# Performance work log

Hardware: AMD Instinct MI355X
Metric: run time of the kernel (lower is better)

The kernel has to match this reference:

```python
import jax, jax.numpy as jnp
import numpy as np


def _pe_2d(H, W, C, dtype):
    # PositionalEncodingPermute2D: returns (C, H, W)
    ch_half = (C + 1) // 2
    inv = 1.0 / (10000.0 ** (jnp.arange(0, ch_half, 2, dtype=jnp.float32) / ch_half))
    tH = jnp.arange(H, dtype=jnp.float32)
    tW = jnp.arange(W, dtype=jnp.float32)
    sinH = tH[:, None] * inv[None, :]              # (H, ch_half//2)
    sinW = tW[:, None] * inv[None, :]              # (W, ch_half//2)
    embH = jnp.concatenate([jnp.sin(sinH), jnp.cos(sinH)], axis=-1)  # (H, ch_half)
    embW = jnp.concatenate([jnp.sin(sinW), jnp.cos(sinW)], axis=-1)  # (W, ch_half)
    E = jnp.concatenate([
        jnp.broadcast_to(embW[None, :, :], (H, W, ch_half)),
        jnp.broadcast_to(embH[:, None, :], (H, W, ch_half)),
    ], axis=-1)[..., :C]                            # (H, W, C)
    return jnp.transpose(E, (2, 0, 1)).astype(dtype)  # (C, H, W)


def setup_inputs() -> dict:
    key = jax.random.key(0)
    k0, k1, k2, k3 = jax.random.split(key, 4)
    B, C, H, W = 4, 256, 64, 64
    s = 1.0 / np.sqrt(C)  # kaiming-ish scale
    return {
        "x": jax.random.normal(k0, (B, C, H, W), dtype=jnp.float32),
        "wq": jax.random.normal(k1, (C, C), dtype=jnp.float32) * s,
        "wk": jax.random.normal(k2, (C, C), dtype=jnp.float32) * s,
        "wv": jax.random.normal(k3, (C, C), dtype=jnp.float32) * s,
    }


def reference(x, wq, wk, wv):
    B, C, H, W = x.shape
    scale = C ** (-0.5)
    x = x + _pe_2d(H, W, C, x.dtype)[None]          # (B, C, H, W)
    X = x.reshape(B, C, H * W).transpose(0, 2, 1)   # (B, N, C)
    Q = jnp.einsum('bnc,dc->bnd', X, wq)
    K = jnp.einsum('bnc,dc->bnd', X, wk)
    V = jnp.einsum('bnc,dc->bnd', X, wv)
    A = jax.nn.softmax(jnp.einsum('bnd,bmd->bnm', Q, K) * scale, axis=-1)
    Y = jnp.einsum('bnm,bmd->bnd', A, V)            # (B, N, C)
    return Y.transpose(0, 2, 1).reshape(B, C, H, W)
```

## Files before the change

### kernel.cpp

```cpp
#include <hip/hip_runtime.h>
#include <hip/hip_bf16.h>

#define BB 4
#define CC 256
#define NN 4096
#define NSPLIT 4
#define KSPLIT (NN / NSPLIT)
#define NPAIR (KSPLIT / 64)

typedef __attribute__((ext_vector_type(8))) short short8;
typedef __attribute__((ext_vector_type(4))) float floatx4;
typedef __attribute__((ext_vector_type(4))) unsigned short ushortx4;

__device__ __forceinline__ float bf2f(unsigned short u) {
  union { unsigned int i; float f; } cv; cv.i = ((unsigned int)u) << 16; return cv.f;
}
__device__ __forceinline__ unsigned short f2bf(float f) {
  union { __hip_bfloat16 h; unsigned short u; } cv; cv.h = __float2bfloat16(f); return cv.u;
}
__device__ __forceinline__ unsigned int cvtpk_bf16(float lo, float hi) {
  unsigned int r;
  asm("v_cvt_pk_bf16_f32 %0, %1, %2" : "=v"(r) : "v"(lo), "v"(hi));
  return r;
}

#define MFMA(a, b, c) __builtin_amdgcn_mfma_f32_16x16x32_bf16((a), (b), (c), 0, 0, 0)

__device__ __forceinline__ void dma16(const unsigned short* g, unsigned short* l) {
  __builtin_amdgcn_global_load_lds(
      (const __attribute__((address_space(1))) unsigned int*)g,
      (__attribute__((address_space(3))) unsigned int*)l, 16, 0, 0);
}
#define S_BARRIER __builtin_amdgcn_s_barrier()
#define MEMFENCE __asm__ volatile("" ::: "memory")

__global__ __launch_bounds__(256) void wcvt(const float* __restrict__ w0,
                                            const float* __restrict__ w1,
                                            const float* __restrict__ w2,
                                            unsigned short* __restrict__ o0,
                                            unsigned short* __restrict__ o1,
                                            unsigned short* __restrict__ o2,
                                            float* __restrict__ PEt) {
  if (blockIdx.y == 3) {
    int idx = blockIdx.x * 256 + threadIdx.x;
    int c = idx >> 6, p = idx & 63, j = c & 63;
    float freq = exp2f(-0.2076205059304601f * (float)j);
    float arg = (float)p * freq;
    PEt[idx] = (c & 64) ? cosf(arg) : sinf(arg);
    return;
  }
  const float* w = (blockIdx.y == 0) ? w0 : (blockIdx.y == 1) ? w1 : w2;
  unsigned short* o = (blockIdx.y == 0) ? o0 : (blockIdx.y == 1) ? o1 : o2;
  float s = (blockIdx.y == 0) ? 0.0901684400555590f : 1.0f;
  int i = (blockIdx.x * 256 + threadIdx.x) * 4;
  floatx4 v = *(const floatx4*)&w[i];
  ushortx4 p;
#pragma unroll
  for (int r = 0; r < 4; r++) p[r] = f2bf(v[r] * s);
  *(ushortx4*)&o[i] = p;
}

__global__ __launch_bounds__(256) void prep_x(const float* __restrict__ x,
                                              const float* __restrict__ PEt,
                                              unsigned short* __restrict__ Xbf) {
  __shared__ float tile[32][33];
  int b = blockIdx.z;
  int n0 = blockIdx.x * 32, c0 = blockIdx.y * 32;
  int tx = threadIdx.x, ty = threadIdx.y;
#pragma unroll
  for (int i = 0; i < 4; i++) {
    int c = c0 + ty + i * 8;
    int n = n0 + tx;
    float v = x[((long)(b * CC + c)) * NN + n];
    int hh = n >> 6, ww = n & 63;
    v += PEt[(c << 6) | ((c < 128) ? ww : hh)];
    tile[ty + i * 8][tx] = v;
  }
  __syncthreads();
#pragma unroll
  for (int i = 0; i < 4; i++) {
    int n = n0 + ty + i * 8;
    int c = c0 + tx;
    Xbf[((long)(b * NN + n)) * CC + c] = f2bf(tile[tx][ty + i * 8]);
  }
}

__global__ __launch_bounds__(256, 2) void gemm_fused(const unsigned short* __restrict__ Xbf,
                                                     const unsigned short* __restrict__ Wqk,
                                                     const unsigned short* __restrict__ Wv,
                                                     unsigned short* __restrict__ QK,
                                                     unsigned short* __restrict__ Vt) {
  __shared__ alignas(16) unsigned short Af[2][8 * 512];
  __shared__ alignas(16) unsigned short Bf[2][8 * 512];
  const unsigned short *Ab, *Bb;
  unsigned short* Ob;
  long row0, col0;
  int ldo;
  int F = blockIdx.x;
  if (F < 512) {
    int b = F >> 7, r = F & 127;
    row0 = (long)(r >> 2) * 128;
    col0 = (long)(r & 3) * 128;
    Ab = Xbf + (long)b * NN * CC;
    Bb = Wqk;
    Ob = QK + (long)b * NN * 512;
    ldo = 512;
  } else {
    int F2 = F - 512;
    int b = F2 >> 6, r = F2 & 63;
    row0 = (long)(r >> 5) * 128;
    col0 = (long)(r & 31) * 128;
    Ab = Wv;
    Bb = Xbf + (long)b * NN * CC;
    Ob = Vt + (long)b * CC * NN;
    ldo = NN;
  }
  int t = threadIdx.x, wave = t >> 6, lane = t & 63, quad = lane >> 4, l15 = lane & 15;
  int wr = wave >> 1, wc = wave & 1;

  auto stage = [&](int k0, int buf) {
#pragma unroll
    for (int i = 0; i < 2; i++) {
      int fg = wave * 2 + i;
      dma16(&Ab[(row0 + fg * 16 + l15) * 256 + k0 + quad * 8], &Af[buf][fg * 512]);
      dma16(&Bb[(col0 + fg * 16 + l15) * 256 + k0 + quad * 8], &Bf[buf][fg * 512]);
    }
  };

  floatx4 acc[4][4] = {};
  stage(0, 0);
  MEMFENCE;
#pragma unroll
  for (int ki = 0; ki < 8; ki++) {
    int buf = ki & 1;
    S_BARRIER;
    MEMFENCE;
    if (ki + 1 < 8) {
      stage((ki + 1) * 32, buf ^ 1);
      MEMFENCE;
      __builtin_amdgcn_s_waitcnt(0xF74);
    } else {
      __builtin_amdgcn_s_waitcnt(0xF70);
    }
    S_BARRIER;
    MEMFENCE;
    short8 af[4], bf[4];
#pragma unroll
    for (int i = 0; i < 4; i++) {
      af[i] = *(const short8*)&Af[buf][(wr * 4 + i) * 512 + lane * 8];
      bf[i] = *(const short8*)&Bf[buf][(wc * 4 + i) * 512 + lane * 8];
    }
#pragma unroll
    for (int i = 0; i < 4; i++)
#pragma unroll
      for (int j = 0; j < 4; j++) acc[i][j] = MFMA(af[i], bf[j], acc[i][j]);
  }

#pragma unroll
  for (int i = 0; i < 4; i++)
#pragma unroll
    for (int j = 0; j < 4; j++) {
      long col = col0 + (wc * 4 + j) * 16 + l15;
#pragma unroll
      for (int r = 0; r < 4; r++) {
        long row = row0 + (wr * 4 + i) * 16 + quad * 4 + r;
        Ob[row * (long)ldo + col] = f2bf(acc[i][j][r]);
      }
    }
}

__global__ __launch_bounds__(512) void attn(const unsigned short* __restrict__ QKg,
                                            const unsigned short* __restrict__ Vtg,
                                            unsigned short* __restrict__ Opart,
                                            float* __restrict__ Lp) {
  __shared__ alignas(16) unsigned short Kl[4 * 8192];
  __shared__ alignas(16) unsigned short Vl[4 * 8192];
  int F = blockIdx.x;
  int c = F & 15, sp = c & 3, b = c >> 2;
  long q0 = (long)(F >> 4) * 256;
  int t = threadIdx.x, wave = t >> 6, lane = t & 63, quad = lane >> 4, l15 = lane & 15;
  const unsigned short* Qb = QKg + (long)b * NN * 512;
  const unsigned short* Kb = Qb + 256;
  const unsigned short* Vb = Vtg + (long)b * CC * NN;

  short8 qf[2][8];
#pragma unroll
  for (int qb = 0; qb < 2; qb++) {
    long qrow = q0 + wave * 32 + qb * 16 + l15;
#pragma unroll
    for (int ks = 0; ks < 8; ks++)
      qf[qb][ks] = *(const short8*)&Qb[qrow * 512 + ks * 32 + quad * 8];
  }

  floatx4 acc[2][16] = {};
  float rs[2] = {0.f, 0.f};

  const int idx0 = (((lane >> 4) & 1) << 7) | ((lane & 15) << 2);
  const int idx1 = idx0 + 64;
  const bool lo32 = lane < 32;

  const int kbeg = sp * KSPLIT;

  auto stage_pair = [&](int p, int buf) {
#pragma unroll
    for (int tt = 0; tt < 2; tt++) {
      int m0 = kbeg + (p * 2 + tt) * 32;
      int slot = buf * 2 + tt;
#pragma unroll
      for (int st = 0; st < 2; st++) {
        int fg = st * 8 + wave;
        dma16(&Kb[(long)(m0 + st * 16 + l15) * 512 + wave * 32 + quad * 8],
              &Kl[slot * 8192 + fg * 512]);
        dma16(&Vb[(long)(fg * 16 + l15) * NN + m0 + quad * 8],
              &Vl[slot * 8192 + fg * 512]);
      }
    }
  };

  __builtin_amdgcn_s_waitcnt(0xF70);
  stage_pair(0, 0);
  MEMFENCE;

  for (int p = 0; p < NPAIR; p++) {
    int buf = p & 1;
    S_BARRIER;
    MEMFENCE;
    if (p + 1 < NPAIR) {
      stage_pair(p + 1, buf ^ 1);
      MEMFENCE;
      __builtin_amdgcn_s_waitcnt(0xF78);
    } else {
      __builtin_amdgcn_s_waitcnt(0xF70);
    }
    S_BARRIER;
    MEMFENCE;

#pragma unroll
    for (int tt = 0; tt < 2; tt++) {
      int kb = (buf * 2 + tt) * 8192;
      floatx4 s2[2][2];
      {
        floatx4 z = {0.f, 0.f, 0.f, 0.f};
        s2[0][0] = z; s2[0][1] = z; s2[1][0] = z; s2[1][1] = z;
      }
      __builtin_amdgcn_s_setprio(1);
#pragma unroll
      for (int fgk = 0; fgk < 16; fgk++) {
        short8 kf = *(const short8*)&Kl[kb + fgk * 512 + lane * 8];
        int mt = fgk >> 3, ks = fgk & 7;
        s2[0][mt] = MFMA(kf, qf[0][ks], s2[0][mt]);
        s2[1][mt] = MFMA(kf, qf[1][ks], s2[1][mt]);
      }
      __builtin_amdgcn_s_setprio(0);

      unsigned int pw[2][2][2];
#pragma unroll
      for (int qb = 0; qb < 2; qb++)
#pragma unroll
        for (int mt = 0; mt < 2; mt++) {
          float e0 = __builtin_amdgcn_exp2f(s2[qb][mt][0]);
          float e1 = __builtin_amdgcn_exp2f(s2[qb][mt][1]);
          float e2 = __builtin_amdgcn_exp2f(s2[qb][mt][2]);
          float e3 = __builtin_amdgcn_exp2f(s2[qb][mt][3]);
          rs[qb] += (e0 + e1) + (e2 + e3);
          pw[qb][mt][0] = cvtpk_bf16(e0, e1);
          pw[qb][mt][1] = cvtpk_bf16(e2, e3);
        }

      short8 pf[2];
#pragma unroll
      for (int qb = 0; qb < 2; qb++) {
        unsigned int x0 = (unsigned int)__builtin_amdgcn_ds_bpermute(idx0, (int)pw[qb][0][0]);
        unsigned int y0 = (unsigned int)__builtin_amdgcn_ds_bpermute(idx0, (int)pw[qb][1][0]);
        unsigned int x1 = (unsigned int)__builtin_amdgcn_ds_bpermute(idx0, (int)pw[qb][0][1]);
        unsigned int y1 = (unsigned int)__builtin_amdgcn_ds_bpermute(idx0, (int)pw[qb][1][1]);
        unsigned int x2 = (unsigned int)__builtin_amdgcn_ds_bpermute(idx1, (int)pw[qb][0][0]);
        unsigned int y2 = (unsigned int)__builtin_amdgcn_ds_bpermute(idx1, (int)pw[qb][1][0]);
        unsigned int x3 = (unsigned int)__builtin_amdgcn_ds_bpermute(idx1, (int)pw[qb][0][1]);
        unsigned int y3 = (unsigned int)__builtin_amdgcn_ds_bpermute(idx1, (int)pw[qb][1][1]);
        union { unsigned int u[4]; short8 s; } pk;
        pk.u[0] = lo32 ? x0 : y0;
        pk.u[1] = lo32 ? x1 : y1;
        pk.u[2] = lo32 ? x2 : y2;
        pk.u[3] = lo32 ? x3 : y3;
        pf[qb] = pk.s;
      }

      __builtin_amdgcn_s_setprio(1);
#pragma unroll
      for (int db = 0; db < 16; db++) {
        short8 vf = *(const short8*)&Vl[kb + db * 512 + lane * 8];
        acc[0][db] = MFMA(pf[0], vf, acc[0][db]);
        acc[1][db] = MFMA(pf[1], vf, acc[1][db]);
      }
      __builtin_amdgcn_s_setprio(0);
    }
  }

  unsigned short* Ob = Opart + (long)(b * NSPLIT + sp) * CC * NN;
#pragma unroll
  for (int qb = 0; qb < 2; qb++) {
    long nidx = q0 + wave * 32 + qb * 16 + quad * 4;
#pragma unroll
    for (int db = 0; db < 16; db++) {
      long d = db * 16 + l15;
      ushortx4 pk;
#pragma unroll
      for (int r = 0; r < 4; r++) pk[r] = f2bf(acc[qb][db][r]);
      *(ushortx4*)&Ob[d * NN + nidx] = pk;
    }
    float v = rs[qb];
    v += __shfl_xor(v, 16, 64);
    v += __shfl_xor(v, 32, 64);
    if (quad == 0)
      Lp[(long)(b * NSPLIT + sp) * NN + q0 + wave * 32 + qb * 16 + l15] = v;
  }
}

__global__ __launch_bounds__(256) void combine(const unsigned short* __restrict__ Op,
                                               const float* __restrict__ Lp,
                                               float* __restrict__ Out) {
  __shared__ float Wl[64];
  int b = blockIdx.z;
  int d0 = blockIdx.y * 64, n0 = blockIdx.x * 64;
  int t = threadIdx.x;
  if (t < 64) {
    int n = n0 + t;
    float L = 0.f;
#pragma unroll
    for (int s = 0; s < NSPLIT; s++) L += Lp[(long)(b * NSPLIT + s) * NN + n];
    Wl[t] = 1.0f / L;
  }
  __syncthreads();
  int tn = t & 15, td = t >> 4;
  int nb = n0 + tn * 4;
  float w[4];
#pragma unroll
  for (int r = 0; r < 4; r++) w[r] = Wl[tn * 4 + r];
#pragma unroll
  for (int dd = 0; dd < 4; dd++) {
    int d = d0 + td * 4 + dd;
    floatx4 o = {0.f, 0.f, 0.f, 0.f};
#pragma unroll
    for (int s = 0; s < NSPLIT; s++) {
      ushortx4 pv = *(const ushortx4*)&Op[((long)(b * NSPLIT + s) * CC + d) * NN + nb];
#pragma unroll
      for (int r = 0; r < 4; r++) o[r] += bf2f(pv[r]);
    }
#pragma unroll
    for (int r = 0; r < 4; r++) o[r] *= w[r];
    *(floatx4*)&Out[((long)b * CC + d) * NN + nb] = o;
  }
}

extern "C" void kernel_launch(void* const* d_in, const int* in_sizes, int n_in,
                              void* d_out, int out_size, void* d_ws, size_t ws_size,
                              hipStream_t stream) {
  const float* x = (const float*)d_in[0];
  const float* wq = (const float*)d_in[1];
  const float* wk = (const float*)d_in[2];
  const float* wv = (const float*)d_in[3];
  float* out = (float*)d_out;

  char* ws = (char*)d_ws;
  unsigned short* QKbuf = (unsigned short*)(ws);
  unsigned short* Vt = (unsigned short*)(ws + (16l << 20));
  unsigned short* Xbf = (unsigned short*)(ws + (24l << 20));
  unsigned short* Opart = (unsigned short*)(ws + (24l << 20));
  float* Lp = (float*)(ws + (56l << 20));
  unsigned short* Wqk = (unsigned short*)(ws + (57l << 20));
  unsigned short* Wv = (unsigned short*)(ws + (57l << 20) + (1 << 19));
  float* PEt = (float*)(ws + (57l << 20) + (3 << 18));

  wcvt<<<dim3(CC * CC / 1024, 4), 256, 0, stream>>>(wq, wk, wv, Wqk, Wqk + CC * CC, Wv, PEt);
  prep_x<<<dim3(NN / 32, CC / 32, BB), dim3(32, 8), 0, stream>>>(x, PEt, Xbf);
  gemm_fused<<<dim3(768), 256, 0, stream>>>(Xbf, Wqk, Wv, QKbuf, Vt);
  attn<<<dim3(256), 512, 0, stream>>>(QKbuf, Vt, Opart, Lp);
  combine<<<dim3(NN / 64, CC / 64, BB), 256, 0, stream>>>(Opart, Lp, out);
}
```

Measured before the change: 191.5 us.

## Split attention into 256-thread blocks of 128 queries with two blocks per CU

The attention kernel now uses 4-wave blocks covering 128 queries instead of 8-wave blocks covering 256. The grid grows to 512 blocks with launch bounds allowing two blocks per CU. Shared memory is halved to a plain double buffer of single 32-key tiles instead of pairs, and each wave stages two K/V fragment groups. Scheduling fences are added around the barriers and waits. The aim is better CU occupancy and overlap across independent blocks, at the cost of loading each K/V tile twice as often from global memory or L2 and tighter register limits.

```diff
diff --git a/kernel.cpp b/kernel.cpp
--- a/kernel.cpp
+++ b/kernel.cpp
@@ -6,7 +6,7 @@
 #define NN 4096
 #define NSPLIT 4
 #define KSPLIT (NN / NSPLIT)
-#define NPAIR (KSPLIT / 64)
+#define NT (KSPLIT / 32)
 
 typedef __attribute__((ext_vector_type(8))) short short8;
 typedef __attribute__((ext_vector_type(4))) float floatx4;
@@ -33,6 +33,7 @@
 }
 #define S_BARRIER __builtin_amdgcn_s_barrier()
 #define MEMFENCE __asm__ volatile("" ::: "memory")
+#define SCHED_FENCE __builtin_amdgcn_sched_barrier(0)
 
 __global__ __launch_bounds__(256) void wcvt(const float* __restrict__ w0,
                                             const float* __restrict__ w1,
@@ -169,15 +170,16 @@
     }
 }
 
-__global__ __launch_bounds__(512) void attn(const unsigned short* __restrict__ QKg,
-                                            const unsigned short* __restrict__ Vtg,
-                                            unsigned short* __restrict__ Opart,
-                                            float* __restrict__ Lp) {
-  __shared__ alignas(16) unsigned short Kl[4 * 8192];
-  __shared__ alignas(16) unsigned short Vl[4 * 8192];
+__global__ __launch_bounds__(256, 2) void attn(const unsigned short* __restrict__ QKg,
+                                               const unsigned short* __restrict__ Vtg,
+                                               unsigned short* __restrict__ Opart,
+                                               float* __restrict__ Lp) {
+  __shared__ alignas(16) unsigned short Kl[2 * 8192];
+  __shared__ alignas(16) unsigned short Vl[2 * 8192];
   int F = blockIdx.x;
-  int c = F & 15, sp = c & 3, b = c >> 2;
-  long q0 = (long)(F >> 4) * 256;
+  int c = F >> 5, qt = F & 31;
+  int sp = c & 3, b = c >> 2;
+  long q0 = (long)qt * 128;
   int t = threadIdx.x, wave = t >> 6, lane = t & 63, quad = lane >> 4, l15 = lane & 15;
   const unsigned short* Qb = QKg + (long)b * NN * 512;
   const unsigned short* Kb = Qb + 256;
@@ -201,100 +203,105 @@
 
   const int kbeg = sp * KSPLIT;
 
-  auto stage_pair = [&](int p, int buf) {
-#pragma unroll
-    for (int tt = 0; tt < 2; tt++) {
-      int m0 = kbeg + (p * 2 + tt) * 32;
-      int slot = buf * 2 + tt;
-#pragma unroll
-      for (int st = 0; st < 2; st++) {
-        int fg = st * 8 + wave;
-        dma16(&Kb[(long)(m0 + st * 16 + l15) * 512 + wave * 32 + quad * 8],
-              &Kl[slot * 8192 + fg * 512]);
+  auto stageT = [&](int tt) {
+    int m0 = kbeg + tt * 32;
+    int kb = (tt & 1) * 8192;
+#pragma unroll
+    for (int st = 0; st < 2; st++) {
+#pragma unroll
+      for (int i = 0; i < 2; i++) {
+        int d = wave * 2 + i;
+        int fg = st * 8 + d;
+        dma16(&Kb[(long)(m0 + st * 16 + l15) * 512 + d * 32 + quad * 8],
+              &Kl[kb + fg * 512]);
         dma16(&Vb[(long)(fg * 16 + l15) * NN + m0 + quad * 8],
-              &Vl[slot * 8192 + fg * 512]);
+              &Vl[kb + fg * 512]);
       }
     }
   };
 
-  __builtin_amdgcn_s_waitcnt(0xF70);
-  stage_pair(0, 0);
   MEMFENCE;
-
-  for (int p = 0; p < NPAIR; p++) {
-    int buf = p & 1;
+  __builtin_amdgcn_s_waitcnt(0x070);
+  SCHED_FENCE;
+  MEMFENCE;
+  stageT(0);
+  MEMFENCE;
+
+#pragma unroll 1
+  for (int tt = 0; tt < NT; tt++) {
     S_BARRIER;
     MEMFENCE;
-    if (p + 1 < NPAIR) {
-      stage_pair(p + 1, buf ^ 1);
+    SCHED_FENCE;
+    if (tt + 1 < NT) {
+      stageT(tt + 1);
       MEMFENCE;
       __builtin_amdgcn_s_waitcnt(0xF78);
     } else {
       __builtin_amdgcn_s_waitcnt(0xF70);
     }
+    SCHED_FENCE;
     S_BARRIER;
     MEMFENCE;
-
-#pragma unroll
-    for (int tt = 0; tt < 2; tt++) {
-      int kb = (buf * 2 + tt) * 8192;
-      floatx4 s2[2][2];
-      {
-        floatx4 z = {0.f, 0.f, 0.f, 0.f};
-        s2[0][0] = z; s2[0][1] = z; s2[1][0] = z; s2[1][1] = z;
+    SCHED_FENCE;
+
+    int kb = (tt & 1) * 8192;
+
+    floatx4 s2[2][2];
+    {
+      floatx4 z = {0.f, 0.f, 0.f, 0.f};
+      s2[0][0] = z; s2[0][1] = z; s2[1][0] = z; s2[1][1] = z;
+    }
+    __builtin_amdgcn_s_setprio(1);
+#pragma unroll
+    for (int fgk = 0; fgk < 16; fgk++) {
+      short8 kf = *(const short8*)&Kl[kb + fgk * 512 + lane * 8];
+      int mt = fgk >> 3, ks = fgk & 7;
+      s2[0][mt] = MFMA(kf, qf[0][ks], s2[0][mt]);
+      s2[1][mt] = MFMA(kf, qf[1][ks], s2[1][mt]);
+    }
+    __builtin_amdgcn_s_setprio(0);
+
+    unsigned int pw[2][2][2];
+#pragma unroll
+    for (int qb = 0; qb < 2; qb++)
+#pragma unroll
+      for (int mt = 0; mt < 2; mt++) {
+        float e0 = __builtin_amdgcn_exp2f(s2[qb][mt][0]);
+        float e1 = __builtin_amdgcn_exp2f(s2[qb][mt][1]);
+        float e2 = __builtin_amdgcn_exp2f(s2[qb][mt][2]);
+        float e3 = __builtin_amdgcn_exp2f(s2[qb][mt][3]);
+        rs[qb] += (e0 + e1) + (e2 + e3);
+        pw[qb][mt][0] = cvtpk_bf16(e0, e1);
+        pw[qb][mt][1] = cvtpk_bf16(e2, e3);
       }
-      __builtin_amdgcn_s_setprio(1);
-#pragma unroll
-      for (int fgk = 0; fgk < 16; fgk++) {
-        short8 kf = *(const short8*)&Kl[kb + fgk * 512 + lane * 8];
-        int mt = fgk >> 3, ks = fgk & 7;
-        s2[0][mt] = MFMA(kf, qf[0][ks], s2[0][mt]);
-        s2[1][mt] = MFMA(kf, qf[1][ks], s2[1][mt]);
-      }
-      __builtin_amdgcn_s_setprio(0);
-
-      unsigned int pw[2][2][2];
-#pragma unroll
-      for (int qb = 0; qb < 2; qb++)
-#pragma unroll
-        for (int mt = 0; mt < 2; mt++) {
-          float e0 = __builtin_amdgcn_exp2f(s2[qb][mt][0]);
-          float e1 = __builtin_amdgcn_exp2f(s2[qb][mt][1]);
-          float e2 = __builtin_amdgcn_exp2f(s2[qb][mt][2]);
-          float e3 = __builtin_amdgcn_exp2f(s2[qb][mt][3]);
-          rs[qb] += (e0 + e1) + (e2 + e3);
-          pw[qb][mt][0] = cvtpk_bf16(e0, e1);
-          pw[qb][mt][1] = cvtpk_bf16(e2, e3);
-        }
-
-      short8 pf[2];
-#pragma unroll
-      for (int qb = 0; qb < 2; qb++) {
-        unsigned int x0 = (unsigned int)__builtin_amdgcn_ds_bpermute(idx0, (int)pw[qb][0][0]);
-        unsigned int y0 = (unsigned int)__builtin_amdgcn_ds_bpermute(idx0, (int)pw[qb][1][0]);
-        unsigned int x1 = (unsigned int)__builtin_amdgcn_ds_bpermute(idx0, (int)pw[qb][0][1]);
-        unsigned int y1 = (unsigned int)__builtin_amdgcn_ds_bpermute(idx0, (int)pw[qb][1][1]);
-        unsigned int x2 = (unsigned int)__builtin_amdgcn_ds_bpermute(idx1, (int)pw[qb][0][0]);
-        unsigned int y2 = (unsigned int)__builtin_amdgcn_ds_bpermute(idx1, (int)pw[qb][1][0]);
-        unsigned int x3 = (unsigned int)__builtin_amdgcn_ds_bpermute(idx1, (int)pw[qb][0][1]);
-        unsigned int y3 = (unsigned int)__builtin_amdgcn_ds_bpermute(idx1, (int)pw[qb][1][1]);
-        union { unsigned int u[4]; short8 s; } pk;
-        pk.u[0] = lo32 ? x0 : y0;
-        pk.u[1] = lo32 ? x1 : y1;
-        pk.u[2] = lo32 ? x2 : y2;
-        pk.u[3] = lo32 ? x3 : y3;
-        pf[qb] = pk.s;
-      }
-
-      __builtin_amdgcn_s_setprio(1);
-#pragma unroll
-      for (int db = 0; db < 16; db++) {
-        short8 vf = *(const short8*)&Vl[kb + db * 512 + lane * 8];
-        acc[0][db] = MFMA(pf[0], vf, acc[0][db]);
-        acc[1][db] = MFMA(pf[1], vf, acc[1][db]);
-      }
-      __builtin_amdgcn_s_setprio(0);
-    }
+
+    short8 pf[2];
+#pragma unroll
+    for (int qb = 0; qb < 2; qb++) {
+      unsigned int x0 = (unsigned int)__builtin_amdgcn_ds_bpermute(idx0, (int)pw[qb][0][0]);
+      unsigned int y0 = (unsigned int)__builtin_amdgcn_ds_bpermute(idx0, (int)pw[qb][1][0]);
+      unsigned int x1 = (unsigned int)__builtin_amdgcn_ds_bpermute(idx0, (int)pw[qb][0][1]);
+      unsigned int y1 = (unsigned int)__builtin_amdgcn_ds_bpermute(idx0, (int)pw[qb][1][1]);
+      unsigned int x2 = (unsigned int)__builtin_amdgcn_ds_bpermute(idx1, (int)pw[qb][0][0]);
+      unsigned int y2 = (unsigned int)__builtin_amdgcn_ds_bpermute(idx1, (int)pw[qb][1][0]);
+      unsigned int x3 = (unsigned int)__builtin_amdgcn_ds_bpermute(idx1, (int)pw[qb][0][1]);
+      unsigned int y3 = (unsigned int)__builtin_amdgcn_ds_bpermute(idx1, (int)pw[qb][1][1]);
+      union { unsigned int u[4]; short8 s; } pk;
+      pk.u[0] = lo32 ? x0 : y0;
+      pk.u[1] = lo32 ? x1 : y1;
+      pk.u[2] = lo32 ? x2 : y2;
+      pk.u[3] = lo32 ? x3 : y3;
+      pf[qb] = pk.s;
+    }
+
+    __builtin_amdgcn_s_setprio(1);
+#pragma unroll
+    for (int db = 0; db < 16; db++) {
+      short8 vf = *(const short8*)&Vl[kb + db * 512 + lane * 8];
+      acc[0][db] = MFMA(pf[0], vf, acc[0][db]);
+      acc[1][db] = MFMA(pf[1], vf, acc[1][db]);
+    }
+    __builtin_amdgcn_s_setprio(0);
   }
 
   unsigned short* Ob = Opart + (long)(b * NSPLIT + sp) * CC * NN;
@@ -375,6 +382,6 @@
   wcvt<<<dim3(CC * CC / 1024, 4), 256, 0, stream>>>(wq, wk, wv, Wqk, Wqk + CC * CC, Wv, PEt);
   prep_x<<<dim3(NN / 32, CC / 32, BB), dim3(32, 8), 0, stream>>>(x, PEt, Xbf);
   gemm_fused<<<dim3(768), 256, 0, stream>>>(Xbf, Wqk, Wv, QKbuf, Vt);
-  attn<<<dim3(256), 512, 0, stream>>>(QKbuf, Vt, Opart, Lp);
+  attn<<<dim3(512), 256, 0, stream>>>(QKbuf, Vt, Opart, Lp);
   combine<<<dim3(NN / 64, CC / 64, BB), 256, 0, stream>>>(Opart, Lp, out);
 }
```

Result: no change. 189.8 us (median of 3 runs) (-0.9%).
